# Kernel optimization log

Hardware: AMD Instinct MI355X
Metric: run time of the kernel (lower is better)

## Reference

```python
import jax, jax.numpy as jnp
import numpy as np

B, T, D = 8, 768, 1024
H = 16
DH = D // H  # 64, RoPE dim per head
ROPE_BASE = 10000.0


def _rope_tables(length, dim, dtype):
    # (T, dim) cos/sin tables, rotate-half convention
    inv_freq = 1.0 / (ROPE_BASE ** (jnp.arange(0, dim, 2, dtype=jnp.float32) / dim))
    ang = jnp.arange(length, dtype=jnp.float32)[:, None] * inv_freq[None, :]  # (T, dim/2)
    cos = jnp.concatenate([jnp.cos(ang), jnp.cos(ang)], axis=-1).astype(dtype)
    sin = jnp.concatenate([jnp.sin(ang), jnp.sin(ang)], axis=-1).astype(dtype)
    return cos, sin


def _rotate_half(x):
    half = x.shape[-1] // 2
    return jnp.concatenate([-x[..., half:], x[..., :half]], axis=-1)


def _apply_rope(x, cos, sin):
    # x: (B, H, T, DH); cos/sin: (T, DH)
    return x * cos[None, None] + _rotate_half(x) * sin[None, None]


def setup_inputs() -> dict:
    key = jax.random.key(0)
    kx, kw, kb = jax.random.split(key, 3)
    x = jax.random.normal(kx, (B, T, D), dtype=jnp.float32)
    bound = 1.0 / np.sqrt(D)
    W_qkv = jax.random.uniform(kw, (3 * D, D), dtype=jnp.float32, minval=-bound, maxval=bound)
    b_qkv = jax.random.uniform(kb, (3 * D,), dtype=jnp.float32, minval=-bound, maxval=bound)
    return {"x": x, "W_qkv": W_qkv, "b_qkv": b_qkv}


def reference(x, W_qkv, b_qkv):
    batch, length, dim = x.shape
    qkv = x @ W_qkv.T + b_qkv                      # (B, T, 3D)
    q, k, v = jnp.split(qkv, 3, axis=-1)
    # (B, T, D) -> (B, H, T, DH)
    def to_heads(t):
        return t.reshape(batch, length, H, DH).transpose(0, 2, 1, 3)
    q, k, v = to_heads(q), to_heads(k), to_heads(v)
    cos, sin = _rope_tables(length, DH, x.dtype)
    q = _apply_rope(q, cos, sin)
    k = _apply_rope(k, cos, sin)
    # parallel retention: QK^T (no softmax, no scale), causal mask multiply, @ V
    scores = jnp.einsum("bhtd,bhsd->bhts", q, k)   # (B, H, T, T)
    mask = jnp.tril(jnp.ones((length, length), dtype=x.dtype))
    retention = scores * mask[None, None]
    out = jnp.einsum("bhts,bhsd->bhtd", retention, v)  # (B, H, T, DH)
    return out.transpose(0, 2, 1, 3).reshape(batch, length, dim)
```

## Files before the change

kernel.cpp:

```cpp
#include <hip/hip_runtime.h>

#define B 8
#define T 768
#define D 1024
#define H 16
#define DH 64
#define M (B*T)
#define N3 (3*D)
#define KDIM D
#define QKV_ELEMS (B*H*T*DH)
#define XE ((size_t)M * KDIM)
#define WE ((size_t)N3 * KDIM)

typedef __attribute__((ext_vector_type(8))) short bf16x8;
typedef __attribute__((ext_vector_type(4))) short bf16x4;
typedef __attribute__((ext_vector_type(4))) float f32x4;

__device__ __forceinline__ unsigned short f2bf(float x) {
    union { float f; unsigned u; } a; a.f = x;
    unsigned r = a.u + 0x7FFFu + ((a.u >> 16) & 1u);
    return (unsigned short)(r >> 16);
}
__device__ __forceinline__ float bf2f(unsigned short h) {
    union { unsigned u; float f; } a; a.u = ((unsigned)h) << 16;
    return a.f;
}

__device__ __forceinline__ void gload_lds16(const void* g, void* l) {
    __builtin_amdgcn_global_load_lds(
        (const __attribute__((address_space(1))) void*)g,
        (__attribute__((address_space(3))) void*)l, 16, 0, 0);
}

__global__ void rope_tables_kernel(float* __restrict__ cosT, float* __restrict__ sinT) {
    int idx = blockIdx.x * blockDim.x + threadIdx.x;
    if (idx >= T * 32) return;
    int t = idx >> 5;
    int i = idx & 31;
    float inv_freq = powf(10000.0f, -(float)(2 * i) / 64.0f);
    float ang = (float)t * inv_freq;
    cosT[idx] = cosf(ang);
    sinT[idx] = sinf(ang);
}

__global__ __launch_bounds__(256) void split_convert_kernel(
    const float* __restrict__ src, unsigned short* __restrict__ hi,
    unsigned short* __restrict__ lo, int n8)
{
    int i = blockIdx.x * blockDim.x + threadIdx.x;
    if (i >= n8) return;
    const float* p = src + (size_t)i * 8;
    float v[8];
    *(float4*)&v[0] = ((const float4*)p)[0];
    *(float4*)&v[4] = ((const float4*)p)[1];
    union { unsigned short u[8]; uint4 q; } hu, lu;
#pragma unroll
    for (int e = 0; e < 8; ++e) {
        unsigned short h = f2bf(v[e]);
        hu.u[e] = h;
        lu.u[e] = f2bf(v[e] - bf2f(h));
    }
    ((uint4*)hi)[i] = hu.q;
    ((uint4*)lo)[i] = lu.q;
}

#define BMq 128
#define BNq 128
#define BKq 32

__global__ __launch_bounds__(256) void qkv_mfma2_kernel(
    const unsigned short* __restrict__ Xhi, const unsigned short* __restrict__ Xlo,
    const unsigned short* __restrict__ Whi, const unsigned short* __restrict__ Wlo,
    const float* __restrict__ bias, const float* __restrict__ cosT,
    const float* __restrict__ sinT, float* __restrict__ qr,
    float* __restrict__ kr, float* __restrict__ vr)
{
    __shared__ unsigned short Ah[BMq * BKq], Al[BMq * BKq];
    __shared__ unsigned short Bh[BNq * BKq], Bl[BNq * BKq];

    const int tid  = threadIdx.x;
    const int lane = tid & 63;
    const int w    = tid >> 6;
    const int wr   = w >> 1;
    const int wc   = w & 1;
    const int lr   = lane & 15;
    const int kc   = lane >> 4;

    const int m0 = blockIdx.x * BMq;
    const int n0 = blockIdx.y * BNq;

    f32x4 acc[4][4];
#pragma unroll
    for (int m = 0; m < 4; ++m)
#pragma unroll
        for (int n = 0; n < 4; ++n) acc[m][n] = (f32x4){0.f, 0.f, 0.f, 0.f};

    for (int k0 = 0; k0 < KDIM; k0 += BKq) {
        __syncthreads();
#pragma unroll
        for (int i = 0; i < 2; ++i) {
            int c   = w * 128 + i * 64 + lane;
            int row = c >> 2;
            int qq  = (c & 3) ^ ((row >> 2) & 3);
            size_t goffA = (size_t)(m0 + row) * KDIM + k0 + qq * 8;
            size_t goffB = (size_t)(n0 + row) * KDIM + k0 + qq * 8;
            int lbase = (w * 128 + i * 64) * 8;
            gload_lds16(Xhi + goffA, &Ah[lbase]);
            gload_lds16(Xlo + goffA, &Al[lbase]);
            gload_lds16(Whi + goffB, &Bh[lbase]);
            gload_lds16(Wlo + goffB, &Bl[lbase]);
        }
        __syncthreads();

        bf16x8 ah[4], al[4], bh[4], bl[4];
#pragma unroll
        for (int m = 0; m < 4; ++m) {
            int r = wr * 64 + m * 16 + lr;
            int idx = r * 32 + (kc ^ ((r >> 2) & 3)) * 8;
            ah[m] = *(const bf16x8*)&Ah[idx];
            al[m] = *(const bf16x8*)&Al[idx];
        }
#pragma unroll
        for (int n = 0; n < 4; ++n) {
            int ccol = wc * 64 + n * 16 + lr;
            int idx = ccol * 32 + (kc ^ ((ccol >> 2) & 3)) * 8;
            bh[n] = *(const bf16x8*)&Bh[idx];
            bl[n] = *(const bf16x8*)&Bl[idx];
        }

#pragma unroll
        for (int m = 0; m < 4; ++m)
#pragma unroll
            for (int n = 0; n < 4; ++n) {
                acc[m][n] = __builtin_amdgcn_mfma_f32_16x16x32_bf16(ah[m], bh[n], acc[m][n], 0, 0, 0);
                acc[m][n] = __builtin_amdgcn_mfma_f32_16x16x32_bf16(ah[m], bl[n], acc[m][n], 0, 0, 0);
                acc[m][n] = __builtin_amdgcn_mfma_f32_16x16x32_bf16(al[m], bh[n], acc[m][n], 0, 0, 0);
            }
    }

    const int section = n0 >> 10;
    float* dst = (section == 0) ? qr : (section == 1) ? kr : vr;
    const int hcol = ((n0 & 1023) >> 6) + wc;

    float biasv[2][2];
#pragma unroll
    for (int np = 0; np < 2; ++np) {
        biasv[np][0] = bias[n0 + wc * 64 + np * 16 + lr];
        biasv[np][1] = bias[n0 + wc * 64 + np * 16 + lr + 32];
    }

#pragma unroll
    for (int m = 0; m < 4; ++m) {
#pragma unroll
        for (int j = 0; j < 4; ++j) {
            int grow = m0 + wr * 64 + m * 16 + (lane >> 4) * 4 + j;
            int bidx = grow / T;
            int t = grow - bidx * T;
            float* rowp = dst + (((size_t)bidx * H + hcol) * T + t) * DH;
#pragma unroll
            for (int np = 0; np < 2; ++np) {
                int d = np * 16 + lr;
                float vlo = acc[m][np][j]     + biasv[np][0];
                float vhi = acc[m][np + 2][j] + biasv[np][1];
                if (section < 2) {
                    float c = cosT[t * 32 + d];
                    float s = sinT[t * 32 + d];
                    float nl = vlo * c - vhi * s;
                    float nh = vhi * c + vlo * s;
                    vlo = nl; vhi = nh;
                }
                rowp[d]      = vlo;
                rowp[d + 32] = vhi;
            }
        }
    }
}

__global__ __launch_bounds__(256) void qkv_mfma_kernel(
    const float* __restrict__ X, const float* __restrict__ W,
    const float* __restrict__ bias, const float* __restrict__ cosT,
    const float* __restrict__ sinT, float* __restrict__ qr,
    float* __restrict__ kr, float* __restrict__ vr)
{
    __shared__ unsigned short Ahi[BMq * BKq];
    __shared__ unsigned short Alo[BMq * BKq];
    __shared__ unsigned short Bhi[BNq * BKq];
    __shared__ unsigned short Blo[BNq * BKq];

    const int tid  = threadIdx.x;
    const int lane = tid & 63;
    const int w    = tid >> 6;
    const int wr   = w >> 1;
    const int wc   = w & 1;
    const int lr   = lane & 15;
    const int kc   = lane >> 4;

    const int m0 = blockIdx.x * BMq;
    const int n0 = blockIdx.y * BNq;

    const int srow = tid >> 1;
    const int kh   = tid & 1;

    f32x4 acc[4][4];
#pragma unroll
    for (int m = 0; m < 4; ++m)
#pragma unroll
        for (int n = 0; n < 4; ++n) acc[m][n] = (f32x4){0.f, 0.f, 0.f, 0.f};

    for (int k0 = 0; k0 < KDIM; k0 += BKq) {
        __syncthreads();
        {
            const float* src = X + (size_t)(m0 + srow) * KDIM + k0 + kh * 16;
            float v[16];
#pragma unroll
            for (int i = 0; i < 4; ++i) ((float4*)v)[i] = ((const float4*)src)[i];
#pragma unroll
            for (int c = 0; c < 2; ++c) {
                int chunk = kh * 2 + c;
                int sidx = srow * 32 + ((chunk ^ ((srow >> 1) & 3)) * 8);
                union { unsigned short u[8]; bf16x8 v8; } hiu, lou;
#pragma unroll
                for (int e = 0; e < 8; ++e) {
                    float x = v[c * 8 + e];
                    unsigned short h = f2bf(x);
                    hiu.u[e] = h;
                    lou.u[e] = f2bf(x - bf2f(h));
                }
                *(bf16x8*)&Ahi[sidx] = hiu.v8;
                *(bf16x8*)&Alo[sidx] = lou.v8;
            }
        }
        {
            const float* src = W + (size_t)(n0 + srow) * KDIM + k0 + kh * 16;
            float v[16];
#pragma unroll
            for (int i = 0; i < 4; ++i) ((float4*)v)[i] = ((const float4*)src)[i];
#pragma unroll
            for (int c = 0; c < 2; ++c) {
                int chunk = kh * 2 + c;
                int sidx = srow * 32 + ((chunk ^ ((srow >> 1) & 3)) * 8);
                union { unsigned short u[8]; bf16x8 v8; } hiu, lou;
#pragma unroll
                for (int e = 0; e < 8; ++e) {
                    float x = v[c * 8 + e];
                    unsigned short h = f2bf(x);
                    hiu.u[e] = h;
                    lou.u[e] = f2bf(x - bf2f(h));
                }
                *(bf16x8*)&Bhi[sidx] = hiu.v8;
                *(bf16x8*)&Blo[sidx] = lou.v8;
            }
        }
        __syncthreads();

        bf16x8 ah[4], al[4], bh[4], bl[4];
#pragma unroll
        for (int m = 0; m < 4; ++m) {
            int row = wr * 64 + m * 16 + lr;
            int idx = row * 32 + ((kc ^ ((row >> 1) & 3)) * 8);
            ah[m] = *(const bf16x8*)&Ahi[idx];
            al[m] = *(const bf16x8*)&Alo[idx];
        }
#pragma unroll
        for (int n = 0; n < 4; ++n) {
            int col = wc * 64 + n * 16 + lr;
            int idx = col * 32 + ((kc ^ ((col >> 1) & 3)) * 8);
            bh[n] = *(const bf16x8*)&Bhi[idx];
            bl[n] = *(const bf16x8*)&Blo[idx];
        }

#pragma unroll
        for (int m = 0; m < 4; ++m)
#pragma unroll
            for (int n = 0; n < 4; ++n) {
                acc[m][n] = __builtin_amdgcn_mfma_f32_16x16x32_bf16(ah[m], bh[n], acc[m][n], 0, 0, 0);
                acc[m][n] = __builtin_amdgcn_mfma_f32_16x16x32_bf16(ah[m], bl[n], acc[m][n], 0, 0, 0);
                acc[m][n] = __builtin_amdgcn_mfma_f32_16x16x32_bf16(al[m], bh[n], acc[m][n], 0, 0, 0);
            }
    }

    const int section = n0 >> 10;
    float* dst = (section == 0) ? qr : (section == 1) ? kr : vr;
    const int hcol = ((n0 & 1023) >> 6) + wc;

    float biasv[2][2];
#pragma unroll
    for (int np = 0; np < 2; ++np) {
        biasv[np][0] = bias[n0 + wc * 64 + np * 16 + lr];
        biasv[np][1] = bias[n0 + wc * 64 + np * 16 + lr + 32];
    }

#pragma unroll
    for (int m = 0; m < 4; ++m) {
#pragma unroll
        for (int j = 0; j < 4; ++j) {
            int grow = m0 + wr * 64 + m * 16 + (lane >> 4) * 4 + j;
            int bidx = grow / T;
            int t = grow - bidx * T;
            float* rowp = dst + (((size_t)bidx * H + hcol) * T + t) * DH;
#pragma unroll
            for (int np = 0; np < 2; ++np) {
                int d = np * 16 + lr;
                float vlo = acc[m][np][j]     + biasv[np][0];
                float vhi = acc[m][np + 2][j] + biasv[np][1];
                if (section < 2) {
                    float c = cosT[t * 32 + d];
                    float s = sinT[t * 32 + d];
                    float nl = vlo * c - vhi * s;
                    float nh = vhi * c + vlo * s;
                    vlo = nl; vhi = nh;
                }
                rowp[d]      = vlo;
                rowp[d + 32] = vhi;
            }
        }
    }
}

#define SBLK 64
#define QBLK 128
#define LDK 72

__global__ __launch_bounds__(256) void retention_mfma_kernel(
    const float* __restrict__ qr, const float* __restrict__ kr,
    const float* __restrict__ vr, float* __restrict__ out)
{
    __shared__ unsigned short Khi[SBLK * LDK], Klo[SBLK * LDK];
    __shared__ unsigned short Vthi[DH * LDK], Vtlo[DH * LDK];
    __shared__ unsigned short Shi[QBLK * LDK], Slo[QBLK * LDK];

    const int qb = blockIdx.x;
    const int bh = blockIdx.y;
    const int b = bh >> 4, h = bh & 15;
    const int tid = threadIdx.x;
    const int lane = tid & 63;
    const int w = tid >> 6;
    const int wm = w >> 1;
    const int wc = w & 1;
    const int lr = lane & 15;
    const int lg = lane >> 4;

    bf16x8 qh[4][2], ql[4][2];
    {
        const float* qp = qr + ((size_t)bh * T + (size_t)qb * QBLK + wm * 64) * DH;
#pragma unroll
        for (int m = 0; m < 4; ++m)
#pragma unroll
            for (int kk = 0; kk < 2; ++kk) {
                const float* p = qp + (m * 16 + lr) * DH + kk * 32 + lg * 8;
                float v[8];
                *(float4*)&v[0] = *(const float4*)p;
                *(float4*)&v[4] = *(const float4*)(p + 4);
                union { unsigned short u[8]; bf16x8 v8; } hu, lu;
#pragma unroll
                for (int e = 0; e < 8; ++e) {
                    unsigned short hv = f2bf(v[e]);
                    hu.u[e] = hv;
                    lu.u[e] = f2bf(v[e] - bf2f(hv));
                }
                qh[m][kk] = hu.v8;
                ql[m][kk] = lu.v8;
            }
    }

    f32x4 oacc[4][2];
#pragma unroll
    for (int m = 0; m < 4; ++m)
#pragma unroll
        for (int n = 0; n < 2; ++n) oacc[m][n] = (f32x4){0.f, 0.f, 0.f, 0.f};

    const int qmin = qb * QBLK + wm * 64;
    const int niter = 2 * qb + 2;

    for (int sb = 0; sb < niter; ++sb) {
        __syncthreads();
        {
            int row = tid >> 2, d0 = (tid & 3) * 16;
            const float* src = kr + ((size_t)bh * T + (size_t)sb * SBLK + row) * DH + d0;
            float v[16];
#pragma unroll
            for (int i = 0; i < 4; ++i) *(float4*)&v[i * 4] = *(const float4*)(src + i * 4);
#pragma unroll
            for (int c = 0; c < 2; ++c) {
                union { unsigned short u[8]; bf16x8 v8; } hu, lu;
#pragma unroll
                for (int e = 0; e < 8; ++e) {
                    float x = v[c * 8 + e];
                    unsigned short hv = f2bf(x);
                    hu.u[e] = hv;
                    lu.u[e] = f2bf(x - bf2f(hv));
                }
                int idx = row * LDK + d0 + c * 8;
                *(bf16x8*)&Khi[idx] = hu.v8;
                *(bf16x8*)&Klo[idx] = lu.v8;
            }
        }
        {
            int s0 = (tid >> 4) * 4, d0 = (tid & 15) * 4;
            const float* src = vr + ((size_t)bh * T + (size_t)sb * SBLK + s0) * DH + d0;
            float rv[4][4];
#pragma unroll
            for (int i = 0; i < 4; ++i) *(float4*)&rv[i][0] = *(const float4*)(src + (size_t)i * DH);
#pragma unroll
            for (int j = 0; j < 4; ++j) {
                union { unsigned short u[4]; bf16x4 v4; } hu, lu;
#pragma unroll
                for (int i = 0; i < 4; ++i) {
                    float x = rv[i][j];
                    unsigned short hv = f2bf(x);
                    hu.u[i] = hv;
                    lu.u[i] = f2bf(x - bf2f(hv));
                }
                int idx = (d0 + j) * LDK + s0;
                *(bf16x4*)&Vthi[idx] = hu.v4;
                *(bf16x4*)&Vtlo[idx] = lu.v4;
            }
        }
        __syncthreads();

        const bool active = (sb * SBLK <= qmin + 63);
        if (active) {
            f32x4 sacc[4][2];
#pragma unroll
            for (int m = 0; m < 4; ++m)
#pragma unroll
                for (int n = 0; n < 2; ++n) sacc[m][n] = (f32x4){0.f, 0.f, 0.f, 0.f};

#pragma unroll
            for (int kk = 0; kk < 2; ++kk) {
                bf16x8 kbh[2], kbl[2];
#pragma unroll
                for (int n = 0; n < 2; ++n) {
                    int s = wc * 32 + n * 16 + lr;
                    int idx = s * LDK + kk * 32 + lg * 8;
                    kbh[n] = *(const bf16x8*)&Khi[idx];
                    kbl[n] = *(const bf16x8*)&Klo[idx];
                }
#pragma unroll
                for (int m = 0; m < 4; ++m)
#pragma unroll
                    for (int n = 0; n < 2; ++n) {
                        sacc[m][n] = __builtin_amdgcn_mfma_f32_16x16x32_bf16(qh[m][kk], kbh[n], sacc[m][n], 0, 0, 0);
                        sacc[m][n] = __builtin_amdgcn_mfma_f32_16x16x32_bf16(qh[m][kk], kbl[n], sacc[m][n], 0, 0, 0);
                        sacc[m][n] = __builtin_amdgcn_mfma_f32_16x16x32_bf16(ql[m][kk], kbh[n], sacc[m][n], 0, 0, 0);
                    }
            }

            const bool needmask = (sb * SBLK + 63 > qmin);
#pragma unroll
            for (int m = 0; m < 4; ++m)
#pragma unroll
                for (int n = 0; n < 2; ++n) {
                    int sl = wc * 32 + n * 16 + lr;
                    int sg = sb * SBLK + sl;
#pragma unroll
                    for (int j = 0; j < 4; ++j) {
                        int rl = wm * 64 + m * 16 + lg * 4 + j;
                        int rg = qb * QBLK + rl;
                        float val = sacc[m][n][j];
                        if (needmask && sg > rg) val = 0.f;
                        unsigned short hv = f2bf(val);
                        int idx = rl * LDK + sl;
                        Shi[idx] = hv;
                        Slo[idx] = f2bf(val - bf2f(hv));
                    }
                }
        }
        __syncthreads();
        if (active) {
#pragma unroll
            for (int kk = 0; kk < 2; ++kk) {
                bf16x8 vbh[2], vbl[2], sah[4], sal[4];
#pragma unroll
                for (int n = 0; n < 2; ++n) {
                    int d = wc * 32 + n * 16 + lr;
                    int idx = d * LDK + kk * 32 + lg * 8;
                    vbh[n] = *(const bf16x8*)&Vthi[idx];
                    vbl[n] = *(const bf16x8*)&Vtlo[idx];
                }
#pragma unroll
                for (int m = 0; m < 4; ++m) {
                    int r = wm * 64 + m * 16 + lr;
                    int idx = r * LDK + kk * 32 + lg * 8;
                    sah[m] = *(const bf16x8*)&Shi[idx];
                    sal[m] = *(const bf16x8*)&Slo[idx];
                }
#pragma unroll
                for (int m = 0; m < 4; ++m)
#pragma unroll
                    for (int n = 0; n < 2; ++n) {
                        oacc[m][n] = __builtin_amdgcn_mfma_f32_16x16x32_bf16(sah[m], vbh[n], oacc[m][n], 0, 0, 0);
                        oacc[m][n] = __builtin_amdgcn_mfma_f32_16x16x32_bf16(sah[m], vbl[n], oacc[m][n], 0, 0, 0);
                        oacc[m][n] = __builtin_amdgcn_mfma_f32_16x16x32_bf16(sal[m], vbh[n], oacc[m][n], 0, 0, 0);
                    }
            }
        }
    }

#pragma unroll
    for (int m = 0; m < 4; ++m)
#pragma unroll
        for (int n = 0; n < 2; ++n) {
            int dcol = wc * 32 + n * 16 + lr;
#pragma unroll
            for (int j = 0; j < 4; ++j) {
                int t = qb * QBLK + wm * 64 + m * 16 + lg * 4 + j;
                out[((size_t)b * T + t) * D + h * DH + dcol] = oacc[m][n][j];
            }
        }
}

extern "C" void kernel_launch(void* const* d_in, const int* in_sizes, int n_in,
                              void* d_out, int out_size, void* d_ws, size_t ws_size,
                              hipStream_t stream) {
    const float* x    = (const float*)d_in[0];
    const float* Wq   = (const float*)d_in[1];
    const float* bq   = (const float*)d_in[2];
    float* out = (float*)d_out;
    float* ws  = (float*)d_ws;

    float* qr   = ws;
    float* kr   = ws + (size_t)QKV_ELEMS;
    float* vr   = ws + (size_t)2 * QKV_ELEMS;
    float* cosT = ws + (size_t)3 * QKV_ELEMS;
    float* sinT = cosT + T * 32;

    const size_t float_bytes = ((size_t)3 * QKV_ELEMS + 2 * T * 32) * sizeof(float);
    unsigned short* Xhi = (unsigned short*)((char*)d_ws + float_bytes);
    unsigned short* Xlo = Xhi + XE;
    unsigned short* Whi = Xlo + XE;
    unsigned short* Wlo = Whi + WE;
    const size_t need = float_bytes + (2 * XE + 2 * WE) * sizeof(unsigned short);

    rope_tables_kernel<<<dim3((T * 32 + 255) / 256), dim3(256), 0, stream>>>(cosT, sinT);

    if (ws_size >= need) {
        split_convert_kernel<<<dim3((int)(XE / 8 / 256)), dim3(256), 0, stream>>>(x,  Xhi, Xlo, (int)(XE / 8));
        split_convert_kernel<<<dim3((int)(WE / 8 / 256)), dim3(256), 0, stream>>>(Wq, Whi, Wlo, (int)(WE / 8));
        qkv_mfma2_kernel<<<dim3(M / BMq, N3 / BNq), dim3(256), 0, stream>>>(
            Xhi, Xlo, Whi, Wlo, bq, cosT, sinT, qr, kr, vr);
    } else {
        qkv_mfma_kernel<<<dim3(M / BMq, N3 / BNq), dim3(256), 0, stream>>>(
            x, Wq, bq, cosT, sinT, qr, kr, vr);
    }

    retention_mfma_kernel<<<dim3(T / QBLK, B * H), dim3(256), 0, stream>>>(qr, kr, vr, out);
}
```

Before: 338.1 us.

## Double-buffer LDS tiles in QKV GEMM and change swizzle pattern

Adds a second LDS buffer for the A/B hi/lo tiles so the next K-slice's global-to-LDS loads are issued before the MFMAs on the current slice, leaving one barrier per iteration instead of two. It also changes the XOR swizzle from row>>2 to row>>1 to reduce LDS bank conflicts on the fragment reads. This doubles LDS use (to 64KB per block), which may reduce occupancy.

```diff
diff --git a/kernel.cpp b/kernel.cpp
--- a/kernel.cpp
+++ b/kernel.cpp
@@ -75,8 +75,8 @@
     const float* __restrict__ sinT, float* __restrict__ qr,
     float* __restrict__ kr, float* __restrict__ vr)
 {
-    __shared__ unsigned short Ah[BMq * BKq], Al[BMq * BKq];
-    __shared__ unsigned short Bh[BNq * BKq], Bl[BNq * BKq];
+    __shared__ unsigned short Ah[2][BMq * BKq], Al[2][BMq * BKq];
+    __shared__ unsigned short Bh[2][BNq * BKq], Bl[2][BNq * BKq];
 
     const int tid  = threadIdx.x;
     const int lane = tid & 63;
@@ -95,37 +95,43 @@
 #pragma unroll
         for (int n = 0; n < 4; ++n) acc[m][n] = (f32x4){0.f, 0.f, 0.f, 0.f};
 
-    for (int k0 = 0; k0 < KDIM; k0 += BKq) {
-        __syncthreads();
+    auto stage = [&](int bufi, int k0s) {
 #pragma unroll
         for (int i = 0; i < 2; ++i) {
             int c   = w * 128 + i * 64 + lane;
             int row = c >> 2;
-            int qq  = (c & 3) ^ ((row >> 2) & 3);
-            size_t goffA = (size_t)(m0 + row) * KDIM + k0 + qq * 8;
-            size_t goffB = (size_t)(n0 + row) * KDIM + k0 + qq * 8;
+            int qq  = (c & 3) ^ ((row >> 1) & 3);
+            size_t goffA = (size_t)(m0 + row) * KDIM + k0s + qq * 8;
+            size_t goffB = (size_t)(n0 + row) * KDIM + k0s + qq * 8;
             int lbase = (w * 128 + i * 64) * 8;
-            gload_lds16(Xhi + goffA, &Ah[lbase]);
-            gload_lds16(Xlo + goffA, &Al[lbase]);
-            gload_lds16(Whi + goffB, &Bh[lbase]);
-            gload_lds16(Wlo + goffB, &Bl[lbase]);
-        }
-        __syncthreads();
+            gload_lds16(Xhi + goffA, &Ah[bufi][lbase]);
+            gload_lds16(Xlo + goffA, &Al[bufi][lbase]);
+            gload_lds16(Whi + goffB, &Bh[bufi][lbase]);
+            gload_lds16(Wlo + goffB, &Bl[bufi][lbase]);
+        }
+    };
+
+    stage(0, 0);
+    __syncthreads();
+    int cur = 0;
+
+    for (int t = 0; t < KDIM / BKq; ++t) {
+        if (t < KDIM / BKq - 1) stage(cur ^ 1, (t + 1) * BKq);
 
         bf16x8 ah[4], al[4], bh[4], bl[4];
 #pragma unroll
         for (int m = 0; m < 4; ++m) {
             int r = wr * 64 + m * 16 + lr;
-            int idx = r * 32 + (kc ^ ((r >> 2) & 3)) * 8;
-            ah[m] = *(const bf16x8*)&Ah[idx];
-            al[m] = *(const bf16x8*)&Al[idx];
+            int idx = r * 32 + (kc ^ ((r >> 1) & 3)) * 8;
+            ah[m] = *(const bf16x8*)&Ah[cur][idx];
+            al[m] = *(const bf16x8*)&Al[cur][idx];
         }
 #pragma unroll
         for (int n = 0; n < 4; ++n) {
             int ccol = wc * 64 + n * 16 + lr;
-            int idx = ccol * 32 + (kc ^ ((ccol >> 2) & 3)) * 8;
-            bh[n] = *(const bf16x8*)&Bh[idx];
-            bl[n] = *(const bf16x8*)&Bl[idx];
+            int idx = ccol * 32 + (kc ^ ((ccol >> 1) & 3)) * 8;
+            bh[n] = *(const bf16x8*)&Bh[cur][idx];
+            bl[n] = *(const bf16x8*)&Bl[cur][idx];
         }
 
 #pragma unroll
@@ -136,6 +142,9 @@
                 acc[m][n] = __builtin_amdgcn_mfma_f32_16x16x32_bf16(ah[m], bl[n], acc[m][n], 0, 0, 0);
                 acc[m][n] = __builtin_amdgcn_mfma_f32_16x16x32_bf16(al[m], bh[n], acc[m][n], 0, 0, 0);
             }
+
+        __syncthreads();
+        cur ^= 1;
     }
 
     const int section = n0 >> 10;
```

New measurement: 358.5 us. 1.06x slower.
